# Optimization experiments

Measured on AMD Instinct MI355X. Metric: run time of the kernel, lower is better.

## Reference

```python
import jax, jax.numpy as jnp
import numpy as np

N_GLOBAL = 100000
N_SUB = 50000
K = 20
IN_DIM = 256
OUT_DIM = 256
EPS = 1e-12  # F.normalize default eps


def setup_inputs() -> dict:
    key = jax.random.key(0)
    k1, k2, k3, k4, k5, k6, k7, k8 = jax.random.split(key, 8)
    X_sub = jax.random.normal(k1, (N_SUB, IN_DIM), dtype=jnp.float32)
    sub_nodes = jax.random.randint(k2, (N_SUB,), 0, N_GLOBAL, dtype=jnp.int64)
    graphsage_nbr_ids = jax.random.randint(k3, (N_GLOBAL, K), 0, N_GLOBAL, dtype=jnp.int64)
    # global->sub map with -1 sentinel for globals not in the subgraph
    global_to_sub = jax.random.randint(k4, (N_GLOBAL,), -1, N_SUB, dtype=jnp.int64)
    # Linear params (torch Linear: y = x @ W.T + b), Kaiming-uniform-ish scale
    s1 = 1.0 / np.sqrt(IN_DIM)
    W_nbr = jax.random.uniform(k5, (OUT_DIM, IN_DIM), jnp.float32, -s1, s1)
    b_nbr = jax.random.uniform(k6, (OUT_DIM,), jnp.float32, -s1, s1)
    s2 = 1.0 / np.sqrt(IN_DIM + OUT_DIM)
    W_final = jax.random.uniform(k7, (OUT_DIM, IN_DIM + OUT_DIM), jnp.float32, -s2, s2)
    b_final = jax.random.uniform(k8, (OUT_DIM,), jnp.float32, -s2, s2)
    return {
        "X_sub": X_sub,
        "sub_nodes": sub_nodes,
        "graphsage_nbr_ids": graphsage_nbr_ids,
        "global_to_sub": global_to_sub,
        "W_nbr": W_nbr,
        "b_nbr": b_nbr,
        "W_final": W_final,
        "b_final": b_final,
    }


def reference(X_sub, sub_nodes, graphsage_nbr_ids, global_to_sub,
              W_nbr, b_nbr, W_final, b_final):
    N_sub = X_sub.shape[0]
    node_expanded = graphsage_nbr_ids[sub_nodes]          # [N_sub, K] global ids
    sub_nbr_indices = global_to_sub[node_expanded]        # [N_sub, K] sub ids or -1
    row_idx = jnp.arange(N_sub)[:, None]                  # [N_sub, 1]
    sub_nbr_indices = jnp.where(sub_nbr_indices < 0, row_idx, sub_nbr_indices)
    nbr_mean = X_sub[sub_nbr_indices].mean(axis=1)        # [N_sub, in_dim]
    h_nbr = jax.nn.relu(nbr_mean @ W_nbr.T + b_nbr)       # [N_sub, out_dim]
    concat_vec = jnp.concatenate([X_sub, h_nbr], axis=1)  # [N_sub, in+out]
    out = jax.nn.relu(concat_vec @ W_final.T + b_final)   # [N_sub, out_dim]
    norm = jnp.linalg.norm(out, axis=1, keepdims=True)
    return out / jnp.maximum(norm, EPS)
```

## Files before the change

### kernel.cpp

```cpp
#include <hip/hip_runtime.h>
#include <hip/hip_bf16.h>

#define KNBR 20
typedef unsigned short u16;
typedef __attribute__((ext_vector_type(8))) short bf16x8;
typedef __attribute__((ext_vector_type(4))) float f32x4;

#define GLDS16(gsrc, ldst)                                                     \
    __builtin_amdgcn_global_load_lds(                                          \
        (const __attribute__((address_space(1))) unsigned int*)(const void*)(gsrc), \
        (__attribute__((address_space(3))) unsigned int*)(void*)(ldst), 16, 0, 0)

__device__ __forceinline__ bool idx_is64(const unsigned int* w) {
    return (w[1] | w[3] | w[5] | w[7] | w[9] | w[11] | w[13] | w[15]) == 0u;
}
__device__ __forceinline__ int idx_at(const int* p, bool is64, long long i) {
    return is64 ? p[2 * i] : p[i];
}
__device__ __forceinline__ u16 f2bf(float x) {
    union { __hip_bfloat16 b; u16 u; } cv;
    cv.b = __float2bfloat16(x);
    return cv.u;
}
__device__ __forceinline__ float blo2f(unsigned int w) {
    union { float f; unsigned int i; } c; c.i = w << 16; return c.f;
}
__device__ __forceinline__ float bhi2f(unsigned int w) {
    union { float f; unsigned int i; } c; c.i = w & 0xffff0000u; return c.f;
}

__global__ void __launch_bounds__(256) k_cast(
    const float* __restrict__ X, const float* __restrict__ Wn,
    const float* __restrict__ Wf, u16* __restrict__ Xb,
    u16* __restrict__ Wnb, u16* __restrict__ Wfb, int nx4)
{
    const int i = blockIdx.x * 256 + threadIdx.x;
    const float4* src; ushort4* dst; int j;
    if (i < nx4)                     { src = (const float4*)X;  dst = (ushort4*)Xb;  j = i; }
    else if (i < nx4 + 16384)        { src = (const float4*)Wn; dst = (ushort4*)Wnb; j = i - nx4; }
    else if (i < nx4 + 16384 + 32768){ src = (const float4*)Wf; dst = (ushort4*)Wfb; j = i - nx4 - 16384; }
    else return;
    const float4 v = src[j];
    ushort4 o;
    o.x = f2bf(v.x); o.y = f2bf(v.y); o.z = f2bf(v.z); o.w = f2bf(v.w);
    dst[j] = o;
}

__global__ void __launch_bounds__(512, 4) k_fused(
    const u16* __restrict__ Xb, const int* __restrict__ sub_nodes,
    const int* __restrict__ nbr, const int* __restrict__ g2s,
    const u16* __restrict__ Wnb, const float* __restrict__ bn,
    const u16* __restrict__ Wfb, const float* __restrict__ bfin,
    float* __restrict__ Out, int M)
{
    __shared__ u16 mh[64 * 256];
    __shared__ u16 Bs[2][256 * 32];
    __shared__ u16 Xs[2][64 * 32];
    __shared__ __align__(16) float sums[64][4];

    const int t    = threadIdx.x;
    const int lane = t & 63;
    const int w    = t >> 6;
    const int wm   = w >> 2;
    const int wn   = w & 3;
    const int l15  = lane & 15;
    const int lk8  = (lane >> 4) << 3;
    const int rsub = (lane >> 4) << 2;
    const int r7   = l15 & 7;
    const int r3   = l15 & 3;
    const int sRow = lane >> 2;
    const int sSlot= lane & 3;
    const int m0   = blockIdx.x * 64;

#define STAGE_B(buf, Bp, KT, tt) do {                                          \
    _Pragma("unroll")                                                          \
    for (int rp_ = 0; rp_ < 2; ++rp_) {                                        \
        const int rr_ = rp_ * 128 + w * 16 + sRow;                             \
        const int cc_ = sSlot ^ (rr_ & 3);                                     \
        GLDS16(Bp + (size_t)rr_ * KT + (tt) * 32 + cc_ * 8,                    \
               &Bs[buf][rp_ * 4096 + w * 512]);                                \
    } } while (0)

#define STAGE_X(buf, tt) do {                                                  \
    if (w < 4) {                                                               \
        const int rl_ = w * 16 + sRow;                                         \
        int rg_ = m0 + rl_; rg_ = (rg_ < M) ? rg_ : (M - 1);                   \
        const int cc_ = sSlot ^ (rl_ & 3);                                     \
        GLDS16(Xb + (size_t)rg_ * 256 + (tt) * 32 + cc_ * 8, &Xs[buf][w * 512]); \
    } } while (0)

    STAGE_B(0, Wnb, 256, 0);

    {
        const bool is64 = idx_is64((const unsigned int*)nbr);
        const int half = lane >> 5;
        const int l31  = lane & 31;
        const int sb   = half << 5;
        #pragma unroll 2
        for (int j = 0; j < 4; ++j) {
            const int rl  = w * 8 + j * 2 + half;
            const int row = m0 + rl;
            const int rowc = (row < M) ? row : (M - 1);
            const int g = idx_at(sub_nodes, is64, rowc);
            int s_my = rowc;
            if (l31 < KNBR) {
                int nid = idx_at(nbr, is64, (long long)g * KNBR + l31);
                int s   = idx_at(g2s, is64, nid);
                s_my = (s < 0) ? rowc : s;
            }
            float a0=0.f,a1=0.f,a2=0.f,a3=0.f,a4=0.f,a5=0.f,a6=0.f,a7=0.f;
            #pragma unroll
            for (int k = 0; k < KNBR; ++k) {
                const int sk = __shfl(s_my, sb + k, 64);
                const uint4 v = *(const uint4*)(Xb + (size_t)sk * 256 + l31 * 8);
                a0 += blo2f(v.x); a1 += bhi2f(v.x);
                a2 += blo2f(v.y); a3 += bhi2f(v.y);
                a4 += blo2f(v.z); a5 += bhi2f(v.z);
                a6 += blo2f(v.w); a7 += bhi2f(v.w);
            }
            const float inv = 1.0f / (float)KNBR;
            uint4 o;
            o.x = (unsigned)f2bf(a0*inv) | ((unsigned)f2bf(a1*inv) << 16);
            o.y = (unsigned)f2bf(a2*inv) | ((unsigned)f2bf(a3*inv) << 16);
            o.z = (unsigned)f2bf(a4*inv) | ((unsigned)f2bf(a5*inv) << 16);
            o.w = (unsigned)f2bf(a6*inv) | ((unsigned)f2bf(a7*inv) << 16);
            *(uint4*)&mh[rl * 256 + ((l31 ^ (rl & 7)) << 3)] = o;
        }
    }
    __syncthreads();

    f32x4 acc[2][4];
    #pragma unroll
    for (int i = 0; i < 2; ++i)
        #pragma unroll
        for (int j = 0; j < 4; ++j)
            acc[i][j] = (f32x4)(0.f);

    #pragma unroll
    for (int tt = 0; tt < 8; ++tt) {
        const int cur = tt & 1;
        if (tt < 7) STAGE_B(cur ^ 1, Wnb, 256, tt + 1);
        bf16x8 af[2], bfr[4];
        #pragma unroll
        for (int fm = 0; fm < 2; ++fm)
            af[fm] = *(const bf16x8*)&mh[(wm*32 + fm*16 + l15) * 256 +
                                         (((tt*4 + (lk8 >> 3)) ^ r7) << 3)];
        #pragma unroll
        for (int fn = 0; fn < 4; ++fn)
            bfr[fn] = *(const bf16x8*)&Bs[cur][(wn*64 + fn*16 + l15) * 32 +
                                              (((lk8 >> 3) ^ r3) << 3)];
        #pragma unroll
        for (int fm = 0; fm < 2; ++fm)
            #pragma unroll
            for (int fn = 0; fn < 4; ++fn)
                acc[fm][fn] = __builtin_amdgcn_mfma_f32_16x16x32_bf16(
                    af[fm], bfr[fn], acc[fm][fn], 0, 0, 0);
        __syncthreads();
    }

    STAGE_B(0, Wfb, 512, 0);
    STAGE_X(0, 0);

    #pragma unroll
    for (int fn = 0; fn < 4; ++fn) {
        const int col = wn * 64 + fn * 16 + l15;
        const float bv = bn[col];
        #pragma unroll
        for (int fm = 0; fm < 2; ++fm)
            #pragma unroll
            for (int r = 0; r < 4; ++r) {
                const int row = wm * 32 + fm * 16 + rsub + r;
                const float v = fmaxf(acc[fm][fn][r] + bv, 0.f);
                mh[row * 256 + ((((col >> 3) ^ (row & 7))) << 3) + (col & 7)] = f2bf(v);
            }
    }
    __syncthreads();

    #pragma unroll
    for (int i = 0; i < 2; ++i)
        #pragma unroll
        for (int j = 0; j < 4; ++j)
            acc[i][j] = (f32x4)(0.f);

    #pragma unroll
    for (int tt = 0; tt < 16; ++tt) {
        const int cur = tt & 1;
        if (tt < 15) {
            STAGE_B(cur ^ 1, Wfb, 512, tt + 1);
            if (tt + 1 < 8) STAGE_X(cur ^ 1, tt + 1);
        }
        bf16x8 af[2], bfr[4];
        if (tt < 8) {
            #pragma unroll
            for (int fm = 0; fm < 2; ++fm)
                af[fm] = *(const bf16x8*)&Xs[cur][(wm*32 + fm*16 + l15) * 32 +
                                                  (((lk8 >> 3) ^ r3) << 3)];
        } else {
            #pragma unroll
            for (int fm = 0; fm < 2; ++fm)
                af[fm] = *(const bf16x8*)&mh[(wm*32 + fm*16 + l15) * 256 +
                                             ((((tt-8)*4 + (lk8 >> 3)) ^ r7) << 3)];
        }
        #pragma unroll
        for (int fn = 0; fn < 4; ++fn)
            bfr[fn] = *(const bf16x8*)&Bs[cur][(wn*64 + fn*16 + l15) * 32 +
                                              (((lk8 >> 3) ^ r3) << 3)];
        #pragma unroll
        for (int fm = 0; fm < 2; ++fm)
            #pragma unroll
            for (int fn = 0; fn < 4; ++fn)
                acc[fm][fn] = __builtin_amdgcn_mfma_f32_16x16x32_bf16(
                    af[fm], bfr[fn], acc[fm][fn], 0, 0, 0);
        __syncthreads();
    }

    float part[2][4];
    #pragma unroll
    for (int fm = 0; fm < 2; ++fm)
        #pragma unroll
        for (int r = 0; r < 4; ++r)
            part[fm][r] = 0.f;
    #pragma unroll
    for (int fn = 0; fn < 4; ++fn) {
        const float bv = bfin[wn * 64 + fn * 16 + l15];
        #pragma unroll
        for (int fm = 0; fm < 2; ++fm)
            #pragma unroll
            for (int r = 0; r < 4; ++r) {
                const float v = fmaxf(acc[fm][fn][r] + bv, 0.f);
                acc[fm][fn][r] = v;
                part[fm][r] += v * v;
            }
    }
    #pragma unroll
    for (int fm = 0; fm < 2; ++fm)
        #pragma unroll
        for (int r = 0; r < 4; ++r) {
            float s = part[fm][r];
            s += __shfl_xor(s, 1, 64);
            s += __shfl_xor(s, 2, 64);
            s += __shfl_xor(s, 4, 64);
            s += __shfl_xor(s, 8, 64);
            part[fm][r] = s;
        }
    if (l15 == 0) {
        #pragma unroll
        for (int fm = 0; fm < 2; ++fm)
            #pragma unroll
            for (int r = 0; r < 4; ++r)
                sums[wm * 32 + fm * 16 + rsub + r][wn] = part[fm][r];
    }
    __syncthreads();
    #pragma unroll
    for (int fm = 0; fm < 2; ++fm)
        #pragma unroll
        for (int r = 0; r < 4; ++r) {
            const int lrow = wm * 32 + fm * 16 + rsub + r;
            const f32x4 sv = *(const f32x4*)&sums[lrow][0];
            const float tot = sv.x + sv.y + sv.z + sv.w;
            const float scale = 1.f / fmaxf(sqrtf(tot), 1e-12f);
            const int row = m0 + lrow;
            if (row < M) {
                #pragma unroll
                for (int fn = 0; fn < 4; ++fn)
                    Out[(size_t)row * 256 + wn * 64 + fn * 16 + l15] =
                        acc[fm][fn][r] * scale;
            }
        }
#undef STAGE_B
#undef STAGE_X
}

extern "C" void kernel_launch(void* const* d_in, const int* in_sizes, int n_in,
                              void* d_out, int out_size, void* d_ws, size_t ws_size,
                              hipStream_t stream)
{
    const float* X         = (const float*)d_in[0];
    const int*   sub_nodes = (const int*)d_in[1];
    const int*   nbr       = (const int*)d_in[2];
    const int*   g2s       = (const int*)d_in[3];
    const float* Wn        = (const float*)d_in[4];
    const float* bn        = (const float*)d_in[5];
    const float* Wf        = (const float*)d_in[6];
    const float* bfin      = (const float*)d_in[7];
    float*       out       = (float*)d_out;

    const int M = out_size / 256;

    u16* Xb  = (u16*)d_ws;
    u16* Wnb = Xb  + (size_t)M * 256;
    u16* Wfb = Wnb + 65536;

    const int nx4 = M * 64;
    const int castTotal = nx4 + 16384 + 32768;
    k_cast<<<(castTotal + 255) / 256, 256, 0, stream>>>(X, Wn, Wf, Xb, Wnb, Wfb, nx4);

    const int fBlocks = (M + 63) / 64;
    k_fused<<<fBlocks, 512, 0, stream>>>(Xb, sub_nodes, nbr, g2s,
                                         Wnb, bn, Wfb, bfin, out, M);
}
```

Before: 125.6 us.

## Reorder phases so X-half of final GEMM runs before gather in alternating blocks

Splits the kernel into phases (gather, X-part of final GEMM, neighbor GEMM, h-part of final GEMM) and keeps two accumulator sets. The X half of the final GEMM no longer depends on h, so it is computed first. Odd blocks do this GEMM work before the gather and even blocks after it, so co-resident blocks mix memory-bound gather with MFMA work. The cost is another 32 accumulator registers per thread, which may lower occupancy, plus more complex staging hand-offs between phases.

```diff
diff --git a/kernel.cpp b/kernel.cpp
--- a/kernel.cpp
+++ b/kernel.cpp
@@ -89,9 +89,16 @@
         GLDS16(Xb + (size_t)rg_ * 256 + (tt) * 32 + cc_ * 8, &Xs[buf][w * 512]); \
     } } while (0)
 
-    STAGE_B(0, Wnb, 256, 0);
-
-    {
+    f32x4 acc1[2][4], acc2[2][4];
+    #pragma unroll
+    for (int i = 0; i < 2; ++i)
+        #pragma unroll
+        for (int j = 0; j < 4; ++j) {
+            acc1[i][j] = (f32x4)(0.f);
+            acc2[i][j] = (f32x4)(0.f);
+        }
+
+    auto PH_G = [&]() {
         const bool is64 = idx_is64((const unsigned int*)nbr);
         const int half = lane >> 5;
         const int l31  = lane & 31;
@@ -126,93 +133,110 @@
             o.w = (unsigned)f2bf(a6*inv) | ((unsigned)f2bf(a7*inv) << 16);
             *(uint4*)&mh[rl * 256 + ((l31 ^ (rl & 7)) << 3)] = o;
         }
-    }
-    __syncthreads();
-
-    f32x4 acc[2][4];
-    #pragma unroll
-    for (int i = 0; i < 2; ++i)
-        #pragma unroll
-        for (int j = 0; j < 4; ++j)
-            acc[i][j] = (f32x4)(0.f);
-
-    #pragma unroll
-    for (int tt = 0; tt < 8; ++tt) {
-        const int cur = tt & 1;
-        if (tt < 7) STAGE_B(cur ^ 1, Wnb, 256, tt + 1);
-        bf16x8 af[2], bfr[4];
-        #pragma unroll
-        for (int fm = 0; fm < 2; ++fm)
-            af[fm] = *(const bf16x8*)&mh[(wm*32 + fm*16 + l15) * 256 +
-                                         (((tt*4 + (lk8 >> 3)) ^ r7) << 3)];
-        #pragma unroll
-        for (int fn = 0; fn < 4; ++fn)
-            bfr[fn] = *(const bf16x8*)&Bs[cur][(wn*64 + fn*16 + l15) * 32 +
-                                              (((lk8 >> 3) ^ r3) << 3)];
-        #pragma unroll
-        for (int fm = 0; fm < 2; ++fm)
+    };
+
+    auto PH_2X = [&]() {
+        #pragma unroll
+        for (int tt = 0; tt < 8; ++tt) {
+            const int cur = tt & 1;
+            if (tt < 7) { STAGE_B(cur ^ 1, Wfb, 512, tt + 1); STAGE_X(cur ^ 1, tt + 1); }
+            else        { STAGE_B(cur ^ 1, Wnb, 256, 0); }
+            bf16x8 af[2], bfr[4];
+            #pragma unroll
+            for (int fm = 0; fm < 2; ++fm)
+                af[fm] = *(const bf16x8*)&Xs[cur][(wm*32 + fm*16 + l15) * 32 +
+                                                  (((lk8 >> 3) ^ r3) << 3)];
             #pragma unroll
             for (int fn = 0; fn < 4; ++fn)
-                acc[fm][fn] = __builtin_amdgcn_mfma_f32_16x16x32_bf16(
-                    af[fm], bfr[fn], acc[fm][fn], 0, 0, 0);
+                bfr[fn] = *(const bf16x8*)&Bs[cur][(wn*64 + fn*16 + l15) * 32 +
+                                                  (((lk8 >> 3) ^ r3) << 3)];
+            #pragma unroll
+            for (int fm = 0; fm < 2; ++fm)
+                #pragma unroll
+                for (int fn = 0; fn < 4; ++fn)
+                    acc2[fm][fn] = __builtin_amdgcn_mfma_f32_16x16x32_bf16(
+                        af[fm], bfr[fn], acc2[fm][fn], 0, 0, 0);
+            __syncthreads();
+        }
+    };
+
+    auto PH_1 = [&]() {
+        #pragma unroll
+        for (int tt = 0; tt < 8; ++tt) {
+            const int cur = tt & 1;
+            if (tt < 7) STAGE_B(cur ^ 1, Wnb, 256, tt + 1);
+            else        STAGE_B(cur ^ 1, Wfb, 512, 8);
+            bf16x8 af[2], bfr[4];
+            #pragma unroll
+            for (int fm = 0; fm < 2; ++fm)
+                af[fm] = *(const bf16x8*)&mh[(wm*32 + fm*16 + l15) * 256 +
+                                             (((tt*4 + (lk8 >> 3)) ^ r7) << 3)];
+            #pragma unroll
+            for (int fn = 0; fn < 4; ++fn)
+                bfr[fn] = *(const bf16x8*)&Bs[cur][(wn*64 + fn*16 + l15) * 32 +
+                                                  (((lk8 >> 3) ^ r3) << 3)];
+            #pragma unroll
+            for (int fm = 0; fm < 2; ++fm)
+                #pragma unroll
+                for (int fn = 0; fn < 4; ++fn)
+                    acc1[fm][fn] = __builtin_amdgcn_mfma_f32_16x16x32_bf16(
+                        af[fm], bfr[fn], acc1[fm][fn], 0, 0, 0);
+            __syncthreads();
+        }
+        #pragma unroll
+        for (int fn = 0; fn < 4; ++fn) {
+            const int col = wn * 64 + fn * 16 + l15;
+            const float bv = bn[col];
+            #pragma unroll
+            for (int fm = 0; fm < 2; ++fm)
+                #pragma unroll
+                for (int r = 0; r < 4; ++r) {
+                    const int row = wm * 32 + fm * 16 + rsub + r;
+                    const float v = fmaxf(acc1[fm][fn][r] + bv, 0.f);
+                    mh[row * 256 + ((((col >> 3) ^ (row & 7))) << 3) + (col & 7)] = f2bf(v);
+                }
+        }
         __syncthreads();
-    }
+    };
+
+    auto PH_2H = [&]() {
+        #pragma unroll
+        for (int tt = 8; tt < 16; ++tt) {
+            const int cur = tt & 1;
+            if (tt < 15) STAGE_B(cur ^ 1, Wfb, 512, tt + 1);
+            bf16x8 af[2], bfr[4];
+            #pragma unroll
+            for (int fm = 0; fm < 2; ++fm)
+                af[fm] = *(const bf16x8*)&mh[(wm*32 + fm*16 + l15) * 256 +
+                                             ((((tt-8)*4 + (lk8 >> 3)) ^ r7) << 3)];
+            #pragma unroll
+            for (int fn = 0; fn < 4; ++fn)
+                bfr[fn] = *(const bf16x8*)&Bs[cur][(wn*64 + fn*16 + l15) * 32 +
+                                                  (((lk8 >> 3) ^ r3) << 3)];
+            #pragma unroll
+            for (int fm = 0; fm < 2; ++fm)
+                #pragma unroll
+                for (int fn = 0; fn < 4; ++fn)
+                    acc2[fm][fn] = __builtin_amdgcn_mfma_f32_16x16x32_bf16(
+                        af[fm], bfr[fn], acc2[fm][fn], 0, 0, 0);
+            __syncthreads();
+        }
+    };
 
     STAGE_B(0, Wfb, 512, 0);
     STAGE_X(0, 0);
-
-    #pragma unroll
-    for (int fn = 0; fn < 4; ++fn) {
-        const int col = wn * 64 + fn * 16 + l15;
-        const float bv = bn[col];
-        #pragma unroll
-        for (int fm = 0; fm < 2; ++fm)
-            #pragma unroll
-            for (int r = 0; r < 4; ++r) {
-                const int row = wm * 32 + fm * 16 + rsub + r;
-                const float v = fmaxf(acc[fm][fn][r] + bv, 0.f);
-                mh[row * 256 + ((((col >> 3) ^ (row & 7))) << 3) + (col & 7)] = f2bf(v);
-            }
+    if (blockIdx.x & 1) {
+        __syncthreads();
+        PH_2X();
+        PH_G();
+        __syncthreads();
+    } else {
+        PH_G();
+        __syncthreads();
+        PH_2X();
     }
-    __syncthreads();
-
-    #pragma unroll
-    for (int i = 0; i < 2; ++i)
-        #pragma unroll
-        for (int j = 0; j < 4; ++j)
-            acc[i][j] = (f32x4)(0.f);
-
-    #pragma unroll
-    for (int tt = 0; tt < 16; ++tt) {
-        const int cur = tt & 1;
-        if (tt < 15) {
-            STAGE_B(cur ^ 1, Wfb, 512, tt + 1);
-            if (tt + 1 < 8) STAGE_X(cur ^ 1, tt + 1);
-        }
-        bf16x8 af[2], bfr[4];
-        if (tt < 8) {
-            #pragma unroll
-            for (int fm = 0; fm < 2; ++fm)
-                af[fm] = *(const bf16x8*)&Xs[cur][(wm*32 + fm*16 + l15) * 32 +
-                                                  (((lk8 >> 3) ^ r3) << 3)];
-        } else {
-            #pragma unroll
-            for (int fm = 0; fm < 2; ++fm)
-                af[fm] = *(const bf16x8*)&mh[(wm*32 + fm*16 + l15) * 256 +
-                                             ((((tt-8)*4 + (lk8 >> 3)) ^ r7) << 3)];
-        }
-        #pragma unroll
-        for (int fn = 0; fn < 4; ++fn)
-            bfr[fn] = *(const bf16x8*)&Bs[cur][(wn*64 + fn*16 + l15) * 32 +
-                                              (((lk8 >> 3) ^ r3) << 3)];
-        #pragma unroll
-        for (int fm = 0; fm < 2; ++fm)
-            #pragma unroll
-            for (int fn = 0; fn < 4; ++fn)
-                acc[fm][fn] = __builtin_amdgcn_mfma_f32_16x16x32_bf16(
-                    af[fm], bfr[fn], acc[fm][fn], 0, 0, 0);
-        __syncthreads();
-    }
+    PH_1();
+    PH_2H();
 
     float part[2][4];
     #pragma unroll
@@ -227,8 +251,8 @@
         for (int fm = 0; fm < 2; ++fm)
             #pragma unroll
             for (int r = 0; r < 4; ++r) {
-                const float v = fmaxf(acc[fm][fn][r] + bv, 0.f);
-                acc[fm][fn][r] = v;
+                const float v = fmaxf(acc2[fm][fn][r] + bv, 0.f);
+                acc2[fm][fn][r] = v;
                 part[fm][r] += v * v;
             }
     }
@@ -264,7 +288,7 @@
                 #pragma unroll
                 for (int fn = 0; fn < 4; ++fn)
                     Out[(size_t)row * 256 + wn * 64 + fn * 16 + l15] =
-                        acc[fm][fn][r] * scale;
+                        acc2[fm][fn][r] * scale;
             }
         }
 #undef STAGE_B
```

Result: slower. 133.5 us (+6.2%).
